# Kernel optimization log

Measured on AMD Instinct MI355X. Metric: run time of the kernel, lower is better.

## Reference

```python
import jax, jax.numpy as jnp
import numpy as np

HIDDEN = 2048
FFN = 2048      # ffn_hidden_size (tp_size == 1)
E = 8           # moe_num_experts
TOP_K = 2       # moe_top_k
S = 2048        # number of tokens


def setup_inputs() -> dict:
    key = jax.random.key(0)
    k1, k2, k3, k4 = jax.random.split(key, 4)
    return {
        "hidden_states": jax.random.normal(k1, (S, HIDDEN), jnp.float32),
        "w_qkv": jax.random.normal(k2, (3 * E, HIDDEN), jnp.float32) * 0.02,
        "w1": jax.random.normal(k3, (E, HIDDEN, 2 * FFN), jnp.float32) * 0.02,
        "w2": jax.random.normal(k4, (E, FFN, HIDDEN), jnp.float32) * 0.02,
        "top_k": TOP_K,
    }


def reference(hidden_states, w_qkv, w1, w2, top_k):
    S, H = hidden_states.shape
    # --- ParallelAttention_router (gate), computed in fp32 as in the source ---
    mix = hidden_states @ w_qkv.T                                  # [S, 3E]
    q, k, v = jnp.split(mix.astype(jnp.float32), 3, axis=-1)       # each [S, E]
    # attn_weights[s,i,j] = q[s,i]*k[s,j]; softmax over j; logits = attn @ v
    attn = jax.nn.softmax(q[:, :, None] * k[:, None, :], axis=-1)  # [S, E, E]
    logits = jnp.einsum('sij,sj->si', attn, v)                     # [S, E]
    # --- top-k routing: softmax over selected logits ---
    top_logits, indices = jax.lax.top_k(logits, top_k)             # [S, K]
    scores = jax.nn.softmax(top_logits, axis=-1).astype(hidden_states.dtype)
    # --- experts: per-expert GLU MLP. The torch code sorts tokens by expert and
    # runs a grouped-GEMM loop; mathematically out[s] = sum_k scores[s,k] *
    # MLP_{indices[s,k]}(x[s]). We compute all experts densely (static shapes)
    # and gather/combine, which is the same math. ---
    fc1 = jnp.einsum('sh,ehi->esi', hidden_states, w1)             # [E, S, 2*FFN]
    g, u = jnp.split(fc1, 2, axis=-1)
    inter = jax.nn.silu(g) * u                                     # [E, S, FFN]
    expert_out = jnp.einsum('esi,eih->esh', inter, w2)             # [E, S, H]
    tok = jnp.arange(S)
    out = jnp.zeros_like(hidden_states)
    for kk in range(top_k):  # tiny static loop over top_k (=2)
        out = out + scores[:, kk, None] * expert_out[indices[:, kk], tok]
    return out
```

## Files before the change

kernel.cpp:

```cpp
#include <hip/hip_runtime.h>
#include <math.h>

#define S_TOK 2048
#define HID   2048
#define FFN_  2048
#define NEXP  8
#define NSLOT (S_TOK*2)

typedef short  s8v __attribute__((ext_vector_type(8)));
typedef short  s4v __attribute__((ext_vector_type(4)));
typedef float  f4v __attribute__((ext_vector_type(4)));

__device__ __forceinline__ unsigned short f32_bf16(float f){
  unsigned u = __float_as_uint(f);
  u += 0x7fffu + ((u>>16)&1u);
  return (unsigned short)(u>>16);
}
__device__ __forceinline__ int lds_off(int r,int kq){
  return (r*4 + (kq ^ ((r>>2)&3)))*8;
}
__device__ __forceinline__ void gl_lds16(const unsigned short* g, unsigned short* l){
  __builtin_amdgcn_global_load_lds(
      (const __attribute__((address_space(1))) unsigned int*)(const void*)g,
      (__attribute__((address_space(3))) unsigned int*)(void*)l,
      16, 0, 0);
}

__global__ void init_k(int* hdr){
  if (threadIdx.x < 24) hdr[threadIdx.x] = 0;
}

__global__ __launch_bounds__(256) void zero_k(float* __restrict__ p){
  int i = (blockIdx.x*256 + threadIdx.x)*4;
  f4v z = {0.f,0.f,0.f,0.f};
  *reinterpret_cast<f4v*>(p + i) = z;
}

__global__ __launch_bounds__(256) void convX_k(
    const float* __restrict__ X, unsigned short* __restrict__ Xb)
{
  int i = (blockIdx.x*256 + threadIdx.x)*8;
  f4v a = *reinterpret_cast<const f4v*>(X + i);
  f4v b = *reinterpret_cast<const f4v*>(X + i + 4);
  s8v o;
  o[0]=(short)f32_bf16(a[0]); o[1]=(short)f32_bf16(a[1]);
  o[2]=(short)f32_bf16(a[2]); o[3]=(short)f32_bf16(a[3]);
  o[4]=(short)f32_bf16(b[0]); o[5]=(short)f32_bf16(b[1]);
  o[6]=(short)f32_bf16(b[2]); o[7]=(short)f32_bf16(b[3]);
  *reinterpret_cast<s8v*>(Xb + i) = o;
}

__global__ __launch_bounds__(256) void transp_k(
    const float* __restrict__ src, unsigned short* __restrict__ dst,
    int K, int N)
{
  const int e = blockIdx.z;
  const int k0 = blockIdx.y*64, n0 = blockIdx.x*128;
  src += (size_t)e*K*N + (size_t)k0*N + n0;
  dst += (size_t)e*N*K + (size_t)n0*K + k0;
  __shared__ __align__(16) unsigned short t[128*66];
  const int tid = threadIdx.x;
  const int nb = tid & 31;
  const int kb = tid >> 5;
  f4v f[8];
  #pragma unroll
  for (int j=0;j<8;j++)
    f[j] = *reinterpret_cast<const f4v*>(src + (size_t)(kb*8+j)*N + nb*4);
  #pragma unroll
  for (int c=0;c<4;c++){
    int n = nb*4 + c;
    s8v v;
    #pragma unroll
    for (int j=0;j<8;j++) v[j] = (short)f32_bf16(f[j][c]);
    *reinterpret_cast<s8v*>(&t[n*66 + ((kb ^ ((n>>5)&3))*8)]) = v;
  }
  __syncthreads();
  #pragma unroll
  for (int p=0;p<4;p++){
    int n = p*32 + (tid>>3);
    int c = tid & 7;
    s8v v = *reinterpret_cast<const s8v*>(&t[n*66 + ((c ^ ((n>>5)&3))*8)]);
    *reinterpret_cast<s8v*>(dst + (size_t)n*K + c*8) = v;
  }
}

__global__ __launch_bounds__(64) void router_k(
    const float* __restrict__ X, const float* __restrict__ Wqkv,
    int* __restrict__ hdr, int* __restrict__ idx, float* __restrict__ scr)
{
  const int s = blockIdx.x, lane = threadIdx.x;
  const float* x = X + (size_t)s*HID;
  f4v xv[8];
  #pragma unroll
  for (int i=0;i<8;i++) xv[i] = *reinterpret_cast<const f4v*>(x + (i*64+lane)*4);
  float dot[24];
  #pragma unroll
  for (int o=0;o<24;o++){
    const float* w = Wqkv + (size_t)o*HID;
    float a = 0.f;
    #pragma unroll
    for (int i=0;i<8;i++){
      f4v wv = *reinterpret_cast<const f4v*>(w + (i*64+lane)*4);
      a += xv[i][0]*wv[0] + xv[i][1]*wv[1] + xv[i][2]*wv[2] + xv[i][3]*wv[3];
    }
    #pragma unroll
    for (int off=32; off; off>>=1) a += __shfl_xor(a, off, 64);
    dot[o] = a;
  }
  if (lane==0){
    float lg[8];
    #pragma unroll
    for (int i=0;i<8;i++){
      float qi = dot[i];
      float mx = -1e30f;
      #pragma unroll
      for (int j=0;j<8;j++) mx = fmaxf(mx, qi*dot[8+j]);
      float se=0.f, lv=0.f;
      #pragma unroll
      for (int j=0;j<8;j++){
        float e = expf(qi*dot[8+j] - mx);
        se += e; lv += e*dot[16+j];
      }
      lg[i] = lv/se;
    }
    int i0=0; float v0=lg[0];
    #pragma unroll
    for (int i=1;i<8;i++) if (lg[i]>v0){v0=lg[i];i0=i;}
    int i1=-1; float v1=-1e30f;
    #pragma unroll
    for (int i=0;i<8;i++) if (i!=i0 && lg[i]>v1){v1=lg[i];i1=i;}
    float a  = expf(v1-v0);
    float s0 = 1.f/(1.f+a);
    idx[s*2]=i0; idx[s*2+1]=i1;
    scr[s*2]=s0; scr[s*2+1]=a*s0;
    atomicAdd(&hdr[i0],1); atomicAdd(&hdr[i1],1);
  }
}

__global__ void scan_k(int* hdr){
  if (threadIdx.x==0){
    int a=0;
    for (int e=0;e<NEXP;e++){ hdr[16+e]=a; a+=hdr[e]; }
  }
}

__global__ __launch_bounds__(256) void scatter_k(
    const int* __restrict__ idx, const float* __restrict__ scr, int* hdr,
    int* __restrict__ tok_slot, float* __restrict__ scr_slot)
{
  int s = blockIdx.x*256 + threadIdx.x;
  if (s >= S_TOK) return;
  #pragma unroll
  for (int k=0;k<2;k++){
    int e    = idx[s*2+k];
    int pos  = atomicAdd(&hdr[8+e], 1);
    int slot = hdr[16+e] + pos;
    tok_slot[slot] = s;
    scr_slot[slot] = scr[s*2+k];
  }
}

__global__ __launch_bounds__(256,3) void gemm1_k(
    const unsigned short* __restrict__ Xb, const unsigned short* __restrict__ W1t,
    const int* __restrict__ hdr, const int* __restrict__ tok_slot,
    unsigned short* __restrict__ inter)
{
  const int e = blockIdx.z, mt = blockIdx.y, nt = blockIdx.x;
  const int cnt = hdr[e];
  const int m0  = mt*128;
  if (m0 >= cnt) return;
  const int off = hdr[16+e];
  const int n0  = nt*64;
  const unsigned short* W1e = W1t + (size_t)e*(2*FFN_)*HID;

  __shared__ __align__(16) unsigned short sA[128*32];
  __shared__ __align__(16) unsigned short sB[128*32];
  __shared__ int sTok[128];

  const int tid = threadIdx.x;
  if (tid < 128){
    int r = m0 + tid; if (r >= cnt) r = cnt-1;
    sTok[tid] = tok_slot[off + r];
  }
  __syncthreads();

  const int lane = tid & 63, wv = tid >> 6;
  const int wm = wv >> 1, wn = wv & 1;
  const int lm = lane & 15, kq = lane >> 4;
  const int srow = lane >> 2, kg = lane & 3;
  const int kgs  = kg ^ (srow >> 2);

  const unsigned short* gA0 = Xb + (size_t)sTok[wv*16 + srow]*HID      + kgs*8;
  const unsigned short* gA1 = Xb + (size_t)sTok[64 + wv*16 + srow]*HID + kgs*8;
  const unsigned short* gB0 = W1e + (size_t)(n0 + wv*16 + srow)*HID        + kgs*8;
  const unsigned short* gB1 = W1e + (size_t)(FFN_ + n0 + wv*16 + srow)*HID + kgs*8;
  unsigned short* lA0 = sA + (wv*16)*32;
  unsigned short* lA1 = sA + (64 + wv*16)*32;
  unsigned short* lB0 = sB + (wv*16)*32;
  unsigned short* lB1 = sB + (64 + wv*16)*32;

  f4v zero = {0.f,0.f,0.f,0.f};
  f4v acc[2][2][4];
  #pragma unroll
  for (int a=0;a<2;a++)
    #pragma unroll
    for (int b=0;b<2;b++)
      #pragma unroll
      for (int c=0;c<4;c++) acc[a][b][c]=zero;

  for (int k0=0; k0<HID; k0+=32){
    gl_lds16(gA0, lA0); gl_lds16(gA1, lA1);
    gl_lds16(gB0, lB0); gl_lds16(gB1, lB1);
    gA0 += 32; gA1 += 32; gB0 += 32; gB1 += 32;
    __syncthreads();
    s8v af[4], bfr[2][2];
    #pragma unroll
    for (int mf=0;mf<4;mf++)
      af[mf] = *reinterpret_cast<const s8v*>(&sA[lds_off(wm*64+mf*16+lm, kq)]);
    #pragma unroll
    for (int st=0; st<2; st++)
      #pragma unroll
      for (int nf=0;nf<2;nf++)
        bfr[st][nf] = *reinterpret_cast<const s8v*>(&sB[lds_off(st*64+wn*32+nf*16+lm, kq)]);
    #pragma unroll
    for (int st=0; st<2; st++)
      #pragma unroll
      for (int nf=0;nf<2;nf++)
        #pragma unroll
        for (int mf=0;mf<4;mf++)
          acc[st][nf][mf] = __builtin_amdgcn_mfma_f32_16x16x32_bf16(
              af[mf], bfr[st][nf], acc[st][nf][mf], 0,0,0);
    __syncthreads();
  }
  const int lq = lane>>4;
  #pragma unroll
  for (int nf=0;nf<2;nf++)
    #pragma unroll
    for (int mf=0;mf<4;mf++){
      f4v g = acc[0][nf][mf], u = acc[1][nf][mf];
      #pragma unroll
      for (int r=0;r<4;r++){
        int row = wm*64 + mf*16 + lq*4 + r;
        if (m0+row < cnt){
          float gv = g[r];
          float val = gv / (1.f + expf(-gv)) * u[r];
          inter[(size_t)(off+m0+row)*FFN_ + n0 + wn*32 + nf*16 + lm] = f32_bf16(val);
        }
      }
    }
}

__global__ __launch_bounds__(256,3) void gemm2_k(
    const unsigned short* __restrict__ inter, const unsigned short* __restrict__ W2t,
    const int* __restrict__ hdr, const int* __restrict__ tok_slot,
    const float* __restrict__ scr_slot, float* __restrict__ out)
{
  const int e = blockIdx.z, mt = blockIdx.y, nt = blockIdx.x;
  const int cnt = hdr[e];
  const int m0  = mt*128;
  if (m0 >= cnt) return;
  const int off = hdr[16+e];
  const int n0  = nt*128;
  const unsigned short* W2e = W2t + (size_t)e*HID*FFN_;

  __shared__ __align__(16) unsigned short sA[128*32];
  __shared__ __align__(16) unsigned short sB[128*32];
  __shared__ int   sTok[128];
  __shared__ float sScr[128];

  const int tid = threadIdx.x;
  if (tid < 128){
    int r = m0 + tid; if (r >= cnt) r = cnt-1;
    sTok[tid] = tok_slot[off + r];
    sScr[tid] = scr_slot[off + r];
  }

  const int lane = tid & 63, wv = tid >> 6;
  const int wm = wv >> 1, wn = wv & 1;
  const int lm = lane & 15, kq = lane >> 4;
  const int srow = lane >> 2, kg = lane & 3;
  const int kgs  = kg ^ (srow >> 2);

  int r0 = m0 + wv*16 + srow;      if (r0 >= cnt) r0 = cnt-1;
  int r1 = m0 + 64 + wv*16 + srow; if (r1 >= cnt) r1 = cnt-1;
  const unsigned short* gA0 = inter + (size_t)(off + r0)*FFN_ + kgs*8;
  const unsigned short* gA1 = inter + (size_t)(off + r1)*FFN_ + kgs*8;
  const unsigned short* gB0 = W2e + (size_t)(n0 + wv*16 + srow)*FFN_      + kgs*8;
  const unsigned short* gB1 = W2e + (size_t)(n0 + 64 + wv*16 + srow)*FFN_ + kgs*8;
  unsigned short* lA0 = sA + (wv*16)*32;
  unsigned short* lA1 = sA + (64 + wv*16)*32;
  unsigned short* lB0 = sB + (wv*16)*32;
  unsigned short* lB1 = sB + (64 + wv*16)*32;

  f4v zero = {0.f,0.f,0.f,0.f};
  f4v acc[4][4];
  #pragma unroll
  for (int a=0;a<4;a++)
    #pragma unroll
    for (int b=0;b<4;b++) acc[a][b]=zero;

  __syncthreads();

  for (int k0=0; k0<FFN_; k0+=32){
    gl_lds16(gA0, lA0); gl_lds16(gA1, lA1);
    gl_lds16(gB0, lB0); gl_lds16(gB1, lB1);
    gA0 += 32; gA1 += 32; gB0 += 32; gB1 += 32;
    __syncthreads();
    s8v af[4], bfr[4];
    #pragma unroll
    for (int mf=0;mf<4;mf++)
      af[mf] = *reinterpret_cast<const s8v*>(&sA[lds_off(wm*64+mf*16+lm, kq)]);
    #pragma unroll
    for (int nf=0;nf<4;nf++)
      bfr[nf] = *reinterpret_cast<const s8v*>(&sB[lds_off(wn*64+nf*16+lm, kq)]);
    #pragma unroll
    for (int nf=0;nf<4;nf++)
      #pragma unroll
      for (int mf=0;mf<4;mf++)
        acc[nf][mf] = __builtin_amdgcn_mfma_f32_16x16x32_bf16(
            af[mf], bfr[nf], acc[nf][mf], 0,0,0);
    __syncthreads();
  }
  const int lq = lane>>4;
  #pragma unroll
  for (int nf=0;nf<4;nf++)
    #pragma unroll
    for (int mf=0;mf<4;mf++)
      #pragma unroll
      for (int r=0;r<4;r++){
        int row = wm*64 + mf*16 + lq*4 + r;
        if (m0+row < cnt)
          atomicAdd(&out[(size_t)sTok[row]*HID + n0 + wn*64 + nf*16 + lm],
                    acc[nf][mf][r]*sScr[row]);
      }
}

extern "C" void kernel_launch(void* const* d_in, const int* in_sizes, int n_in,
                              void* d_out, int out_size, void* d_ws, size_t ws_size,
                              hipStream_t stream)
{
  const float* X    = (const float*)d_in[0];
  const float* Wqkv = (const float*)d_in[1];
  const float* W1   = (const float*)d_in[2];
  const float* W2   = (const float*)d_in[3];
  float* out = (float*)d_out;

  char* ws = (char*)d_ws;
  int*   hdr      = (int*)ws;
  int*   idx      = (int*)(ws + 4096);
  float* scr      = (float*)(ws + 4096 + 1*16384);
  int*   tok_slot = (int*)(ws + 4096 + 2*16384);
  float* scr_slot = (float*)(ws + 4096 + 3*16384);
  size_t o = 4096 + 4*16384;
  unsigned short* Xb    = (unsigned short*)(ws + o); o += (size_t)S_TOK*HID*2;
  unsigned short* inter = (unsigned short*)(ws + o); o += (size_t)NSLOT*FFN_*2;
  unsigned short* W1t   = (unsigned short*)(ws + o); o += (size_t)NEXP*2*FFN_*HID*2;
  unsigned short* W2t   = (unsigned short*)(ws + o);

  init_k   <<<1,   64, 0, stream>>>(hdr);
  zero_k   <<<(S_TOK*HID/4)/256, 256, 0, stream>>>(out);
  convX_k  <<<(S_TOK*HID/8)/256, 256, 0, stream>>>(X, Xb);
  transp_k <<<dim3((2*FFN_)/128, HID/64, NEXP), 256, 0, stream>>>(W1, W1t, HID, 2*FFN_);
  transp_k <<<dim3(HID/128,     FFN_/64, NEXP), 256, 0, stream>>>(W2, W2t, FFN_, HID);

  router_k <<<S_TOK,64,0, stream>>>(X, Wqkv, hdr, idx, scr);
  scan_k   <<<1,   64, 0, stream>>>(hdr);
  scatter_k<<<(S_TOK+255)/256, 256, 0, stream>>>(idx, scr, hdr, tok_slot, scr_slot);
  gemm1_k  <<<dim3(FFN_/64,  S_TOK/128, NEXP), 256, 0, stream>>>(Xb, W1t, hdr, tok_slot, inter);
  gemm2_k  <<<dim3(HID/128,  S_TOK/128, NEXP), 256, 0, stream>>>(inter, W2t, hdr, tok_slot, scr_slot, out);
}
```

Measured before the change: 789.3 us.

## Fuse prep kernels, drop scan/scatter via per-expert capacity slots, swizzle GEMM grids

Result: no change. 777.4 us (-1.5%).

```diff
diff --git a/kernel.cpp b/kernel.cpp
--- a/kernel.cpp
+++ b/kernel.cpp
@@ -5,7 +5,7 @@
 #define HID   2048
 #define FFN_  2048
 #define NEXP  8
-#define NSLOT (S_TOK*2)
+#define CAP   2048
 
 typedef short  s8v __attribute__((ext_vector_type(8)));
 typedef short  s4v __attribute__((ext_vector_type(4)));
@@ -26,40 +26,46 @@
       16, 0, 0);
 }
 
-__global__ void init_k(int* hdr){
-  if (threadIdx.x < 24) hdr[threadIdx.x] = 0;
-}
-
-__global__ __launch_bounds__(256) void zero_k(float* __restrict__ p){
-  int i = (blockIdx.x*256 + threadIdx.x)*4;
-  f4v z = {0.f,0.f,0.f,0.f};
-  *reinterpret_cast<f4v*>(p + i) = z;
-}
-
-__global__ __launch_bounds__(256) void convX_k(
-    const float* __restrict__ X, unsigned short* __restrict__ Xb)
-{
-  int i = (blockIdx.x*256 + threadIdx.x)*8;
-  f4v a = *reinterpret_cast<const f4v*>(X + i);
-  f4v b = *reinterpret_cast<const f4v*>(X + i + 4);
-  s8v o;
-  o[0]=(short)f32_bf16(a[0]); o[1]=(short)f32_bf16(a[1]);
-  o[2]=(short)f32_bf16(a[2]); o[3]=(short)f32_bf16(a[3]);
-  o[4]=(short)f32_bf16(b[0]); o[5]=(short)f32_bf16(b[1]);
-  o[6]=(short)f32_bf16(b[2]); o[7]=(short)f32_bf16(b[3]);
-  *reinterpret_cast<s8v*>(Xb + i) = o;
-}
-
-__global__ __launch_bounds__(256) void transp_k(
-    const float* __restrict__ src, unsigned short* __restrict__ dst,
-    int K, int N)
-{
-  const int e = blockIdx.z;
-  const int k0 = blockIdx.y*64, n0 = blockIdx.x*128;
+__global__ __launch_bounds__(256) void prep_k(
+    const float* __restrict__ X,  unsigned short* __restrict__ Xb,
+    const float* __restrict__ W1, unsigned short* __restrict__ W1t,
+    const float* __restrict__ W2, unsigned short* __restrict__ W2t,
+    float* __restrict__ out, int* __restrict__ hdr)
+{
+  const int bid = blockIdx.x, tid = threadIdx.x;
+  __shared__ __align__(16) unsigned short t[128*66];
+
+  if (bid < 4096){
+    if (bid==0 && tid<8) hdr[tid] = 0;
+    int i = (bid*256 + tid)*4;
+    f4v z = {0.f,0.f,0.f,0.f};
+    *reinterpret_cast<f4v*>(out + i) = z;
+    return;
+  }
+  if (bid < 6144){
+    int i = ((bid-4096)*256 + tid)*8;
+    f4v a = *reinterpret_cast<const f4v*>(X + i);
+    f4v b = *reinterpret_cast<const f4v*>(X + i + 4);
+    s8v o;
+    o[0]=(short)f32_bf16(a[0]); o[1]=(short)f32_bf16(a[1]);
+    o[2]=(short)f32_bf16(a[2]); o[3]=(short)f32_bf16(a[3]);
+    o[4]=(short)f32_bf16(b[0]); o[5]=(short)f32_bf16(b[1]);
+    o[6]=(short)f32_bf16(b[2]); o[7]=(short)f32_bf16(b[3]);
+    *reinterpret_cast<s8v*>(Xb + i) = o;
+    return;
+  }
+  const float* src; unsigned short* dst; int K,N,n0,k0,e;
+  if (bid < 14336){
+    int b = bid - 6144; e = b>>10; int rem = b&1023;
+    N = 4096; K = 2048; n0 = (rem&31)*128; k0 = (rem>>5)*64;
+    src = W1; dst = W1t;
+  } else {
+    int b = bid - 14336; e = b>>9; int rem = b&511;
+    N = 2048; K = 2048; n0 = (rem&15)*128; k0 = (rem>>4)*64;
+    src = W2; dst = W2t;
+  }
   src += (size_t)e*K*N + (size_t)k0*N + n0;
   dst += (size_t)e*N*K + (size_t)n0*K + k0;
-  __shared__ __align__(16) unsigned short t[128*66];
-  const int tid = threadIdx.x;
   const int nb = tid & 31;
   const int kb = tid >> 5;
   f4v f[8];
@@ -86,7 +92,7 @@
 
 __global__ __launch_bounds__(64) void router_k(
     const float* __restrict__ X, const float* __restrict__ Wqkv,
-    int* __restrict__ hdr, int* __restrict__ idx, float* __restrict__ scr)
+    int* __restrict__ hdr, int* __restrict__ tok_slot, float* __restrict__ scr_slot)
 {
   const int s = blockIdx.x, lane = threadIdx.x;
   const float* x = X + (size_t)s*HID;
@@ -131,32 +137,10 @@
     for (int i=0;i<8;i++) if (i!=i0 && lg[i]>v1){v1=lg[i];i1=i;}
     float a  = expf(v1-v0);
     float s0 = 1.f/(1.f+a);
-    idx[s*2]=i0; idx[s*2+1]=i1;
-    scr[s*2]=s0; scr[s*2+1]=a*s0;
-    atomicAdd(&hdr[i0],1); atomicAdd(&hdr[i1],1);
-  }
-}
-
-__global__ void scan_k(int* hdr){
-  if (threadIdx.x==0){
-    int a=0;
-    for (int e=0;e<NEXP;e++){ hdr[16+e]=a; a+=hdr[e]; }
-  }
-}
-
-__global__ __launch_bounds__(256) void scatter_k(
-    const int* __restrict__ idx, const float* __restrict__ scr, int* hdr,
-    int* __restrict__ tok_slot, float* __restrict__ scr_slot)
-{
-  int s = blockIdx.x*256 + threadIdx.x;
-  if (s >= S_TOK) return;
-  #pragma unroll
-  for (int k=0;k<2;k++){
-    int e    = idx[s*2+k];
-    int pos  = atomicAdd(&hdr[8+e], 1);
-    int slot = hdr[16+e] + pos;
-    tok_slot[slot] = s;
-    scr_slot[slot] = scr[s*2+k];
+    int p0 = atomicAdd(&hdr[i0],1);
+    int p1 = atomicAdd(&hdr[i1],1);
+    tok_slot[i0*CAP+p0] = s;  scr_slot[i0*CAP+p0] = s0;
+    tok_slot[i1*CAP+p1] = s;  scr_slot[i1*CAP+p1] = a*s0;
   }
 }
 
@@ -165,11 +149,13 @@
     const int* __restrict__ hdr, const int* __restrict__ tok_slot,
     unsigned short* __restrict__ inter)
 {
-  const int e = blockIdx.z, mt = blockIdx.y, nt = blockIdx.x;
+  const int bid = blockIdx.x;
+  const int swz = (bid&7)*512 + (bid>>3);
+  const int e = swz>>9, rem = swz&511, nt = rem>>4, mt = rem&15;
   const int cnt = hdr[e];
   const int m0  = mt*128;
   if (m0 >= cnt) return;
-  const int off = hdr[16+e];
+  const int off = e*CAP;
   const int n0  = nt*64;
   const unsigned short* W1e = W1t + (size_t)e*(2*FFN_)*HID;
 
@@ -188,7 +174,7 @@
   const int wm = wv >> 1, wn = wv & 1;
   const int lm = lane & 15, kq = lane >> 4;
   const int srow = lane >> 2, kg = lane & 3;
-  const int kgs  = kg ^ (srow >> 2);
+  const int kgs  = kg ^ ((srow >> 2)&3);
 
   const unsigned short* gA0 = Xb + (size_t)sTok[wv*16 + srow]*HID      + kgs*8;
   const unsigned short* gA1 = Xb + (size_t)sTok[64 + wv*16 + srow]*HID + kgs*8;
@@ -255,11 +241,13 @@
     const int* __restrict__ hdr, const int* __restrict__ tok_slot,
     const float* __restrict__ scr_slot, float* __restrict__ out)
 {
-  const int e = blockIdx.z, mt = blockIdx.y, nt = blockIdx.x;
+  const int bid = blockIdx.x;
+  const int swz = (bid&7)*256 + (bid>>3);
+  const int e = swz>>8, rem = swz&255, nt = rem>>4, mt = rem&15;
   const int cnt = hdr[e];
   const int m0  = mt*128;
   if (m0 >= cnt) return;
-  const int off = hdr[16+e];
+  const int off = e*CAP;
   const int n0  = nt*128;
   const unsigned short* W2e = W2t + (size_t)e*HID*FFN_;
 
@@ -279,7 +267,7 @@
   const int wm = wv >> 1, wn = wv & 1;
   const int lm = lane & 15, kq = lane >> 4;
   const int srow = lane >> 2, kg = lane & 3;
-  const int kgs  = kg ^ (srow >> 2);
+  const int kgs  = kg ^ ((srow >> 2)&3);
 
   int r0 = m0 + wv*16 + srow;      if (r0 >= cnt) r0 = cnt-1;
   int r1 = m0 + 64 + wv*16 + srow; if (r1 >= cnt) r1 = cnt-1;
@@ -347,25 +335,16 @@
 
   char* ws = (char*)d_ws;
   int*   hdr      = (int*)ws;
-  int*   idx      = (int*)(ws + 4096);
-  float* scr      = (float*)(ws + 4096 + 1*16384);
-  int*   tok_slot = (int*)(ws + 4096 + 2*16384);
-  float* scr_slot = (float*)(ws + 4096 + 3*16384);
-  size_t o = 4096 + 4*16384;
+  int*   tok_slot = (int*)(ws + 4096);
+  float* scr_slot = (float*)(ws + 4096 + 65536);
+  size_t o = 4096 + 2*65536;
   unsigned short* Xb    = (unsigned short*)(ws + o); o += (size_t)S_TOK*HID*2;
-  unsigned short* inter = (unsigned short*)(ws + o); o += (size_t)NSLOT*FFN_*2;
+  unsigned short* inter = (unsigned short*)(ws + o); o += (size_t)NEXP*CAP*FFN_*2;
   unsigned short* W1t   = (unsigned short*)(ws + o); o += (size_t)NEXP*2*FFN_*HID*2;
   unsigned short* W2t   = (unsigned short*)(ws + o);
 
-  init_k   <<<1,   64, 0, stream>>>(hdr);
-  zero_k   <<<(S_TOK*HID/4)/256, 256, 0, stream>>>(out);
-  convX_k  <<<(S_TOK*HID/8)/256, 256, 0, stream>>>(X, Xb);
-  transp_k <<<dim3((2*FFN_)/128, HID/64, NEXP), 256, 0, stream>>>(W1, W1t, HID, 2*FFN_);
-  transp_k <<<dim3(HID/128,     FFN_/64, NEXP), 256, 0, stream>>>(W2, W2t, FFN_, HID);
-
-  router_k <<<S_TOK,64,0, stream>>>(X, Wqkv, hdr, idx, scr);
-  scan_k   <<<1,   64, 0, stream>>>(hdr);
-  scatter_k<<<(S_TOK+255)/256, 256, 0, stream>>>(idx, scr, hdr, tok_slot, scr_slot);
-  gemm1_k  <<<dim3(FFN_/64,  S_TOK/128, NEXP), 256, 0, stream>>>(Xb, W1t, hdr, tok_slot, inter);
-  gemm2_k  <<<dim3(HID/128,  S_TOK/128, NEXP), 256, 0, stream>>>(inter, W2t, hdr, tok_slot, scr_slot, out);
-}
+  prep_k   <<<18432, 256, 0, stream>>>(X, Xb, W1, W1t, W2, W2t, out, hdr);
+  router_k <<<S_TOK, 64,  0, stream>>>(X, Wqkv, hdr, tok_slot, scr_slot);
+  gemm1_k  <<<4096,  256, 0, stream>>>(Xb, W1t, hdr, tok_slot, inter);
+  gemm2_k  <<<2048,  256, 0, stream>>>(inter, W2t, hdr, tok_slot, scr_slot, out);
+}
```
